# Optimization experiments

Hardware: AMD Instinct MI355X
Metric: run time of the kernel (lower is better)

Reference implementation:

```python
import jax, jax.numpy as jnp
import numpy as np

N_HEAD = 16
N_KV_HEAD = 4
HEAD_DIM = 64
VE_CH = 12  # min(12, n_embd)


def apply_rotary_emb(x, cos, sin):
    d = x.shape[3] // 2
    x1, x2 = x[..., :d], x[..., d:]
    return jnp.concatenate([x1 * cos + x2 * sin, x1 * -sin + x2 * cos], axis=3)


def rms_norm(x):
    return x * jax.lax.rsqrt(jnp.mean(jnp.square(x), axis=-1, keepdims=True) + 1e-6)


def setup_inputs() -> dict:
    key = jax.random.key(0)
    ks = jax.random.split(key, 9)
    B, T, C = 2, 2048, 1024
    s = 0.02
    return {
        "x": jax.random.normal(ks[0], (B, T, C), jnp.float32),
        "ve": jax.random.normal(ks[1], (B, T, N_KV_HEAD * HEAD_DIM), jnp.float32),
        "cos": jax.random.normal(ks[2], (1, T, 1, HEAD_DIM // 2), jnp.float32),
        "sin": jax.random.normal(ks[3], (1, T, 1, HEAD_DIM // 2), jnp.float32),
        "Wq": jax.random.normal(ks[4], (C, C), jnp.float32) * s,
        "Wk": jax.random.normal(ks[5], (N_KV_HEAD * HEAD_DIM, C), jnp.float32) * s,
        "Wv": jax.random.normal(ks[6], (N_KV_HEAD * HEAD_DIM, C), jnp.float32) * s,
        "Wo": jax.random.normal(ks[7], (C, C), jnp.float32) * s,
        "Wg": jax.random.normal(ks[8], (N_KV_HEAD, VE_CH), jnp.float32) * s,
    }


def reference(x, ve, cos, sin, Wq, Wk, Wv, Wo, Wg):
    B, T, C = x.shape
    q = (x @ Wq.T).reshape(B, T, N_HEAD, HEAD_DIM)
    k = (x @ Wk.T).reshape(B, T, N_KV_HEAD, HEAD_DIM)
    v = (x @ Wv.T).reshape(B, T, N_KV_HEAD, HEAD_DIM)

    # value-embedding gate
    ve_r = ve.reshape(B, T, N_KV_HEAD, HEAD_DIM)
    gate = 3.0 * jax.nn.sigmoid(x[..., :VE_CH] @ Wg.T)  # [B,T,n_kv_head]
    v = v + gate[..., None] * ve_r

    q = apply_rotary_emb(q, cos, sin)
    k = apply_rotary_emb(k, cos, sin)
    q = rms_norm(q) * 1.2
    k = rms_norm(k) * 1.2

    # GQA: expand kv heads
    r = N_HEAD // N_KV_HEAD
    k = jnp.repeat(k, r, axis=2)
    v = jnp.repeat(v, r, axis=2)

    # [B,H,T,D]
    q = q.transpose(0, 2, 1, 3)
    k = k.transpose(0, 2, 1, 3)
    v = v.transpose(0, 2, 1, 3)

    scale = 1.0 / np.sqrt(HEAD_DIM).astype(np.float32)
    scores = jnp.einsum("bhqd,bhkd->bhqk", q, k) * scale
    causal = jnp.tril(jnp.ones((T, T), dtype=bool))
    scores = jnp.where(causal, scores, jnp.float32(-jnp.inf))
    att = jax.nn.softmax(scores, axis=-1)
    y = jnp.einsum("bhqk,bhkd->bhqd", att, v)
    y = y.transpose(0, 2, 1, 3).reshape(B, T, C)
    return y @ Wo.T
```

## Files before the change

### kernel.cpp

```cpp
#include <hip/hip_runtime.h>
#include <stdint.h>

#define B_SZ 2
#define T_SZ 2048
#define C_SZ 1024
#define NH   16
#define NKV  4
#define HD   64
#define KVD  256
#define QKV_N 1536

typedef __attribute__((ext_vector_type(8))) short bf16x8;
typedef __attribute__((ext_vector_type(4))) float f32x4;

#define GL(p) ((const __attribute__((address_space(1))) void*)(p))
#define LD(p) ((__attribute__((address_space(3))) void*)(p))

__device__ inline unsigned short f2bf(float f) {
  union { float f; unsigned u; } v; v.f = f;
  unsigned u = v.u;
  unsigned r = (u + 0x7fffu + ((u >> 16) & 1u)) >> 16;
  return (unsigned short)r;
}
__device__ inline unsigned short bftrunc(float f) {
  union { float f; unsigned u; } v; v.f = f;
  return (unsigned short)(v.u >> 16);
}

struct CvtArgs {
  const float *s0, *s1, *s2, *s3, *s4;
  unsigned short *d0, *d1, *d2, *d3, *d4;
  const float *x, *Wg;
  float *gate;
};
__global__ __launch_bounds__(256) void cvt_all(CvtArgs a) {
  int blk = blockIdx.x, tid = threadIdx.x;
  if (blk >= 6656) {
    int idx = (blk - 6656) * 256 + tid;
    int bt = idx >> 2, kh = idx & 3;
    float s = 0.f;
#pragma unroll
    for (int j = 0; j < 12; j++) s += a.x[(size_t)bt * C_SZ + j] * a.Wg[kh * 12 + j];
    a.gate[idx] = 3.f / (1.f + __expf(-s));
    return;
  }
  const float* s; unsigned short* d; int i;
  if      (blk < 4096) { s = a.s0; d = a.d0; i = blk * 256 + tid; }
  else if (blk < 5120) { s = a.s1; d = a.d1; i = (blk - 4096) * 256 + tid; }
  else if (blk < 5376) { s = a.s2; d = a.d2; i = (blk - 5120) * 256 + tid; }
  else if (blk < 5632) { s = a.s3; d = a.d3; i = (blk - 5376) * 256 + tid; }
  else                 { s = a.s4; d = a.d4; i = (blk - 5632) * 256 + tid; }
  float4 f = ((const float4*)s)[i];
  ushort4 o;
  o.x = f2bf(f.x); o.y = f2bf(f.y); o.z = f2bf(f.z); o.w = f2bf(f.w);
  ((ushort4*)d)[i] = o;
}

#define GEMM_PROLOG(A, Bm, K)                                                        \
  __shared__ unsigned short As[2][64 * 64];                                          \
  __shared__ unsigned short Bs[2][128 * 64];                                         \
  int tid  = threadIdx.x;                                                            \
  int lane = tid & 63;                                                               \
  int wave = tid >> 6;                                                               \
  int quad = lane >> 4;                                                              \
  int l16  = lane & 15;                                                              \
  int m0 = blockIdx.y * 64;                                                          \
  int n0 = blockIdx.x * 128;                                                         \
  int wm = (wave & 1) * 32;                                                          \
  int wn = (wave >> 1) * 64;                                                         \
  f32x4 acc[2][4];                                                                   \
  _Pragma("unroll") for (int i = 0; i < 2; i++)                                      \
    _Pragma("unroll") for (int j = 0; j < 4; j++)                                    \
      acc[i][j] = (f32x4){0.f, 0.f, 0.f, 0.f};                                       \
  int lrow = lane >> 3;                                 \
  int lcol = ((lane & 7) ^ lrow) * 8;                 \
  int sA = wave * 16;                                                                \
  int sB = wave * 32;                                                                \
  const unsigned short* aP0 = &A[(size_t)(m0 + sA + lrow) * K + lcol];               \
  const unsigned short* aP1 = aP0 + 8 * (size_t)K;                                   \
  const unsigned short* bP0 = &Bm[(size_t)(n0 + sB + lrow) * K + lcol];              \
  const unsigned short* bP1 = bP0 + 8 * (size_t)K;                                   \
  const unsigned short* bP2 = bP0 + 16 * (size_t)K;                                  \
  const unsigned short* bP3 = bP0 + 24 * (size_t)K;                                  \
  __builtin_amdgcn_global_load_lds(GL(aP0), LD(&As[0][(sA     ) * 64]), 16, 0, 0);   \
  __builtin_amdgcn_global_load_lds(GL(aP1), LD(&As[0][(sA +  8) * 64]), 16, 0, 0);   \
  __builtin_amdgcn_global_load_lds(GL(bP0), LD(&Bs[0][(sB     ) * 64]), 16, 0, 0);   \
  __builtin_amdgcn_global_load_lds(GL(bP1), LD(&Bs[0][(sB +  8) * 64]), 16, 0, 0);   \
  __builtin_amdgcn_global_load_lds(GL(bP2), LD(&Bs[0][(sB + 16) * 64]), 16, 0, 0);   \
  __builtin_amdgcn_global_load_lds(GL(bP3), LD(&Bs[0][(sB + 24) * 64]), 16, 0, 0);   \
  int swz = l16 & 7;                                                                 \
  int nk = K >> 6;                                                                   \
  for (int ki = 0; ki < nk; ki++) {                                                  \
    int cur = ki & 1, nxt = cur ^ 1;                                                 \
    __syncthreads();                                                                 \
    if (ki + 1 < nk) {                                                               \
      int k0 = (ki + 1) << 6;                                                        \
      __builtin_amdgcn_global_load_lds(GL(aP0 + k0), LD(&As[nxt][(sA     ) * 64]), 16, 0, 0); \
      __builtin_amdgcn_global_load_lds(GL(aP1 + k0), LD(&As[nxt][(sA +  8) * 64]), 16, 0, 0); \
      __builtin_amdgcn_global_load_lds(GL(bP0 + k0), LD(&Bs[nxt][(sB     ) * 64]), 16, 0, 0); \
      __builtin_amdgcn_global_load_lds(GL(bP1 + k0), LD(&Bs[nxt][(sB +  8) * 64]), 16, 0, 0); \
      __builtin_amdgcn_global_load_lds(GL(bP2 + k0), LD(&Bs[nxt][(sB + 16) * 64]), 16, 0, 0); \
      __builtin_amdgcn_global_load_lds(GL(bP3 + k0), LD(&Bs[nxt][(sB + 24) * 64]), 16, 0, 0); \
    }                                                                                \
    _Pragma("unroll") for (int p = 0; p < 2; p++) {                                  \
      bf16x8 af[2], bfr[4];                                                          \
      _Pragma("unroll") for (int i = 0; i < 2; i++)                                  \
        af[i] = *(const bf16x8*)&As[cur][(wm + i * 16 + l16) * 64 + (((p * 4 + quad) ^ swz) * 8)]; \
      _Pragma("unroll") for (int j = 0; j < 4; j++)                                  \
        bfr[j] = *(const bf16x8*)&Bs[cur][(wn + j * 16 + l16) * 64 + (((p * 4 + quad) ^ swz) * 8)]; \
      _Pragma("unroll") for (int i = 0; i < 2; i++)                                  \
        _Pragma("unroll") for (int j = 0; j < 4; j++)                                \
          acc[i][j] = __builtin_amdgcn_mfma_f32_16x16x32_bf16(af[i], bfr[j], acc[i][j], 0, 0, 0); \
    }                                                                                \
  }

__global__ __launch_bounds__(256) void gemm_bt(const unsigned short* __restrict__ A,
                                               const unsigned short* __restrict__ Bm,
                                               float* __restrict__ C,
                                               int N, int K) {
  GEMM_PROLOG(A, Bm, K)
#pragma unroll
  for (int i = 0; i < 2; i++) {
#pragma unroll
    for (int j = 0; j < 4; j++) {
      int col = n0 + wn + j * 16 + l16;
#pragma unroll
      for (int r = 0; r < 4; r++) {
        int row = m0 + wm + i * 16 + quad * 4 + r;
        C[(size_t)row * N + col] = acc[i][j][r];
      }
    }
  }
}

__global__ __launch_bounds__(256) void gemm_qkv(const unsigned short* __restrict__ A,
                                                const unsigned short* __restrict__ Bm,
                                                const float* __restrict__ ve,
                                                const float* __restrict__ cosb,
                                                const float* __restrict__ sinb,
                                                const float* __restrict__ gateArr,
                                                unsigned short* __restrict__ qa,
                                                unsigned short* __restrict__ ka,
                                                unsigned short* __restrict__ vt) {
  const int K = C_SZ;
  GEMM_PROLOG(A, Bm, K)

  int colbase = n0 + wn;
  if (colbase < 1280) {
    int isQ = colbase < 1024;
    int h   = isQ ? (colbase >> 6) : ((colbase - 1024) >> 6);
    float scale = isQ ? (0.15f * 1.44269504088896f) : 1.2f;
    unsigned short* dst = isQ ? qa : ka;
    int nheads = isQ ? NH : NKV;
#pragma unroll
    for (int i = 0; i < 2; i++) {
#pragma unroll
      for (int r = 0; r < 4; r++) {
        int row = m0 + wm + i * 16 + quad * 4 + r;
        int t = row & (T_SZ - 1), b = row >> 11;
        float a10 = acc[i][0][r], a11 = acc[i][1][r];
        float a20 = acc[i][2][r], a21 = acc[i][3][r];
        float cv0 = cosb[t * 32 + l16],      sv0 = sinb[t * 32 + l16];
        float cv1 = cosb[t * 32 + 16 + l16], sv1 = sinb[t * 32 + 16 + l16];
        float o10 =  a10 * cv0 + a20 * sv0;
        float o11 =  a11 * cv1 + a21 * sv1;
        float o20 = -a10 * sv0 + a20 * cv0;
        float o21 = -a11 * sv1 + a21 * cv1;
        float ssq = o10 * o10 + o11 * o11 + o20 * o20 + o21 * o21;
        ssq += __shfl_xor(ssq, 1);
        ssq += __shfl_xor(ssq, 2);
        ssq += __shfl_xor(ssq, 4);
        ssq += __shfl_xor(ssq, 8);
        float rn = rsqrtf(ssq * (1.f / 64.f) + 1e-6f) * scale;
        size_t base = ((size_t)(b * nheads + h) * T_SZ + t) * HD;
        dst[base + l16]      = f2bf(o10 * rn);
        dst[base + 16 + l16] = f2bf(o11 * rn);
        dst[base + 32 + l16] = f2bf(o20 * rn);
        dst[base + 48 + l16] = f2bf(o21 * rn);
      }
    }
  } else {
    int kh  = (colbase - 1280) >> 6;
    int khb = (n0 - 1280) >> 6;
    unsigned short* tile = (unsigned short*)&Bs[0][0];
    const int TS = 132;
#pragma unroll
    for (int i = 0; i < 2; i++) {
#pragma unroll
      for (int r = 0; r < 4; r++) {
        int rl  = wm + i * 16 + quad * 4 + r;
        int row = m0 + rl;
        float g = gateArr[row * 4 + kh];
#pragma unroll
        for (int j = 0; j < 4; j++) {
          int d = j * 16 + l16;
          float val = acc[i][j][r] + g * ve[(size_t)row * KVD + kh * HD + d];
          tile[rl * TS + wn + d] = f2bf(val);
        }
      }
    }
    __syncthreads();
    int d2  = tid & 127;
    int seg = tid >> 7;
    int khw = khb + (d2 >> 6);
    int dd  = d2 & 63;
    int bb  = m0 >> 11;
    int tl0 = (m0 & (T_SZ - 1)) + seg * 32;
    unsigned short* dstp = &vt[((size_t)(bb * NKV + khw) * HD + dd) * T_SZ + tl0];
#pragma unroll
    for (int k4 = 0; k4 < 8; k4++) {
      ushort4 o;
      o.x = tile[(seg * 32 + k4 * 4 + 0) * TS + d2];
      o.y = tile[(seg * 32 + k4 * 4 + 1) * TS + d2];
      o.z = tile[(seg * 32 + k4 * 4 + 2) * TS + d2];
      o.w = tile[(seg * 32 + k4 * 4 + 3) * TS + d2];
      *(ushort4*)(dstp + k4 * 4) = o;
    }
  }
}

#define KST 72
#define PST 72
__global__ __launch_bounds__(512, 4) void attn(const unsigned short* __restrict__ qa,
                                               const unsigned short* __restrict__ ka,
                                               const unsigned short* __restrict__ vt,
                                               unsigned short* __restrict__ y) {
  int bid = blockIdx.x;
  int half = bid >> 8, r = bid & 255;
  int qt = half ? (r & 15) : 15 - (r & 15);
  int bh = (half << 4) | (r >> 4);
  int b = bh >> 4, h = bh & 15;
  int kh = h >> 2;
  int tid = threadIdx.x;
  int wave = tid >> 6, lane = tid & 63;
  int quad = lane >> 4, l16 = lane & 15;

  __shared__ unsigned short Ks[2][64 * KST];
  __shared__ unsigned short Vs[2][64 * KST];
  __shared__ unsigned short Ps[128 * PST];
  unsigned short* Pw = &Ps[(wave * 16) * PST];

  int qrow0 = qt * 128 + wave * 16;

  bf16x8 bq0, bq1;
  {
    int tq = qrow0 + l16;
    const unsigned short* qp = &qa[((size_t)(b * NH + h) * T_SZ + tq) * HD];
    bq0 = *(const bf16x8*)&qp[quad * 8];
    bq1 = *(const bf16x8*)&qp[32 + quad * 8];
  }

  const unsigned short one_bf = 0x3F80;
  bf16x8 vones = {(short)one_bf, (short)one_bf, (short)one_bf, (short)one_bf,
                  (short)one_bf, (short)one_bf, (short)one_bf, (short)one_bf};

  f32x4 oacc[4];
  f32x4 lacc = (f32x4){0.f, 0.f, 0.f, 0.f};
#pragma unroll
  for (int d = 0; d < 4; d++) oacc[d] = (f32x4){0.f, 0.f, 0.f, 0.f};

  int lr = tid >> 3;
  int lc = (tid & 7) * 8;

  const unsigned short* kbase = &ka[(size_t)(b * NKV + kh) * T_SZ * HD];
  const unsigned short* vbase = &vt[(size_t)(b * NKV + kh) * HD * T_SZ];

  int nj = 2 * qt + 2;

  {
    uint4 k0 = *(const uint4*)&kbase[(size_t)lr * HD + lc];
    uint4 v0 = *(const uint4*)&vbase[(size_t)lr * T_SZ + lc];
    *(uint4*)&Ks[0][lr * KST + lc] = k0;
    *(uint4*)&Vs[0][lr * KST + lc] = v0;
  }

  for (int j = 0; j < nj; j++) {
    int cur = j & 1, nxt = cur ^ 1;
    __syncthreads();

    uint4 k0, v0;
    bool pf = (j + 1 < nj);
    if (pf) {
      k0 = *(const uint4*)&kbase[(size_t)((j + 1) * 64 + lr) * HD + lc];
      v0 = *(const uint4*)&vbase[(size_t)lr * T_SZ + (j + 1) * 64 + lc];
    }

    bool active = (j * 64) <= (qrow0 + 15);

    if (active) {
      f32x4 st[4];
      __builtin_amdgcn_s_setprio(1);
#pragma unroll
      for (int tb = 0; tb < 4; tb++) {
        bf16x8 ak0 = *(const bf16x8*)&Ks[cur][(tb * 16 + l16) * KST + quad * 8];
        bf16x8 ak1 = *(const bf16x8*)&Ks[cur][(tb * 16 + l16) * KST + 32 + quad * 8];
        f32x4 s = (f32x4){0.f, 0.f, 0.f, 0.f};
        s = __builtin_amdgcn_mfma_f32_16x16x32_bf16(ak0, bq0, s, 0, 0, 0);
        s = __builtin_amdgcn_mfma_f32_16x16x32_bf16(ak1, bq1, s, 0, 0, 0);
        st[tb] = s;
      }
      __builtin_amdgcn_s_setprio(0);

      if (j * 64 + 63 > qrow0) {
        int qg = qrow0 + l16;
#pragma unroll
        for (int tb = 0; tb < 4; tb++) {
          int tg = j * 64 + tb * 16 + quad * 4;
#pragma unroll
          for (int i = 0; i < 4; i++) {
            if (tg + i > qg) st[tb][i] = -__builtin_inff();
          }
        }
      }
#pragma unroll
      for (int tb = 0; tb < 4; tb++) {
        ushort4 w;
        w.x = bftrunc(__builtin_amdgcn_exp2f(st[tb][0]));
        w.y = bftrunc(__builtin_amdgcn_exp2f(st[tb][1]));
        w.z = bftrunc(__builtin_amdgcn_exp2f(st[tb][2]));
        w.w = bftrunc(__builtin_amdgcn_exp2f(st[tb][3]));
        *(ushort4*)&Pw[l16 * PST + tb * 16 + quad * 4] = w;
      }

      bf16x8 ap0 = *(const bf16x8*)&Pw[l16 * PST + quad * 8];
      bf16x8 ap1 = *(const bf16x8*)&Pw[l16 * PST + 32 + quad * 8];
      __builtin_amdgcn_s_setprio(1);
      lacc = __builtin_amdgcn_mfma_f32_16x16x32_bf16(ap0, vones, lacc, 0, 0, 0);
      lacc = __builtin_amdgcn_mfma_f32_16x16x32_bf16(ap1, vones, lacc, 0, 0, 0);
#pragma unroll
      for (int d = 0; d < 4; d++) {
        bf16x8 bv0 = *(const bf16x8*)&Vs[cur][(d * 16 + l16) * KST + quad * 8];
        bf16x8 bv1 = *(const bf16x8*)&Vs[cur][(d * 16 + l16) * KST + 32 + quad * 8];
        oacc[d] = __builtin_amdgcn_mfma_f32_16x16x32_bf16(ap0, bv0, oacc[d], 0, 0, 0);
        oacc[d] = __builtin_amdgcn_mfma_f32_16x16x32_bf16(ap1, bv1, oacc[d], 0, 0, 0);
      }
      __builtin_amdgcn_s_setprio(0);
    }

    if (pf) {
      *(uint4*)&Ks[nxt][lr * KST + lc] = k0;
      *(uint4*)&Vs[nxt][lr * KST + lc] = v0;
    }
  }

#pragma unroll
  for (int i = 0; i < 4; i++) {
    int tq = qrow0 + quad * 4 + i;
    float inv = 1.f / lacc[i];
#pragma unroll
    for (int d = 0; d < 4; d++) {
      y[((size_t)(b * T_SZ) + tq) * C_SZ + h * HD + d * 16 + l16] = f2bf(oacc[d][i] * inv);
    }
  }
}

extern "C" void kernel_launch(void* const* d_in, const int* in_sizes, int n_in,
                              void* d_out, int out_size, void* d_ws, size_t ws_size,
                              hipStream_t stream) {
  const float* x    = (const float*)d_in[0];
  const float* ve   = (const float*)d_in[1];
  const float* cosb = (const float*)d_in[2];
  const float* sinb = (const float*)d_in[3];
  const float* Wq   = (const float*)d_in[4];
  const float* Wk   = (const float*)d_in[5];
  const float* Wv   = (const float*)d_in[6];
  const float* Wo   = (const float*)d_in[7];
  const float* Wg   = (const float*)d_in[8];
  float* out = (float*)d_out;

  const size_t MB = 1024 * 1024;
  char* ws = (char*)d_ws;
  unsigned short* xb    = (unsigned short*)(ws);
  unsigned short* wqkvb = (unsigned short*)(ws + 8 * MB);
  unsigned short* wob   = (unsigned short*)(ws + 11 * MB);
  unsigned short* qab   = (unsigned short*)(ws + 13 * MB);
  unsigned short* kab   = (unsigned short*)(ws + 21 * MB);
  unsigned short* vtb   = (unsigned short*)(ws + 23 * MB);
  float*          gateA = (float*)(ws + 25 * MB);
  unsigned short* yb    = xb;

  CvtArgs ca;
  ca.s0 = x;  ca.d0 = xb;
  ca.s1 = Wq; ca.d1 = wqkvb;
  ca.s2 = Wk; ca.d2 = wqkvb + 1024 * 1024;
  ca.s3 = Wv; ca.d3 = wqkvb + 1280 * 1024;
  ca.s4 = Wo; ca.d4 = wob;
  ca.x = x; ca.Wg = Wg; ca.gate = gateA;
  cvt_all<<<6720, 256, 0, stream>>>(ca);

  gemm_qkv<<<dim3(QKV_N / 128, (B_SZ * T_SZ) / 64), 256, 0, stream>>>(
      xb, wqkvb, ve, cosb, sinb, gateA, qab, kab, vtb);

  attn<<<512, 512, 0, stream>>>(qab, kab, vtb, yb);

  gemm_bt<<<dim3(C_SZ / 128, (B_SZ * T_SZ) / 64), 256, 0, stream>>>(
      yb, wob, out, C_SZ, C_SZ);
}
```

Before: 161.4 us.

## Switch attention to 32x32 MFMA with register-resident P via permlane swap

Rewrites the attention kernel so each wave handles 32 query rows with 32x32x16 bf16 MFMAs instead of 16x16x32. The softmax probabilities stay in registers: they are packed with v_cvt_pk_bf16_f32 and rearranged with v_permlane32_swap, which removes the per-wave LDS round trip for P. The row sum is now accumulated in scalar adds instead of an MFMA against a ones vector. Blocks drop to 256 threads (4 waves) with the same 128-query tile, which raises per-thread register use and removes the occupancy hint.

```diff
diff --git a/kernel.cpp b/kernel.cpp
--- a/kernel.cpp
+++ b/kernel.cpp
@@ -12,6 +12,7 @@
 
 typedef __attribute__((ext_vector_type(8))) short bf16x8;
 typedef __attribute__((ext_vector_type(4))) float f32x4;
+typedef __attribute__((ext_vector_type(16))) float f32x16;
 
 #define GL(p) ((const __attribute__((address_space(1))) void*)(p))
 #define LD(p) ((__attribute__((address_space(3))) void*)(p))
@@ -22,9 +23,10 @@
   unsigned r = (u + 0x7fffu + ((u >> 16) & 1u)) >> 16;
   return (unsigned short)r;
 }
-__device__ inline unsigned short bftrunc(float f) {
-  union { float f; unsigned u; } v; v.f = f;
-  return (unsigned short)(v.u >> 16);
+__device__ inline unsigned cvtpk_bf16(float lo, float hi_) {
+  unsigned r;
+  asm("v_cvt_pk_bf16_f32 %0, %1, %2" : "=v"(r) : "v"(lo), "v"(hi_));
+  return r;
 }
 
 struct CvtArgs {
@@ -220,11 +222,10 @@
 }
 
 #define KST 72
-#define PST 72
-__global__ __launch_bounds__(512, 4) void attn(const unsigned short* __restrict__ qa,
-                                               const unsigned short* __restrict__ ka,
-                                               const unsigned short* __restrict__ vt,
-                                               unsigned short* __restrict__ y) {
+__global__ __launch_bounds__(256) void attn(const unsigned short* __restrict__ qa,
+                                            const unsigned short* __restrict__ ka,
+                                            const unsigned short* __restrict__ vt,
+                                            unsigned short* __restrict__ y) {
   int bid = blockIdx.x;
   int half = bid >> 8, r = bid & 255;
   int qt = half ? (r & 15) : 15 - (r & 15);
@@ -233,34 +234,30 @@
   int kh = h >> 2;
   int tid = threadIdx.x;
   int wave = tid >> 6, lane = tid & 63;
-  int quad = lane >> 4, l16 = lane & 15;
+  int l32 = lane & 31, hi = lane >> 5;
 
   __shared__ unsigned short Ks[2][64 * KST];
   __shared__ unsigned short Vs[2][64 * KST];
-  __shared__ unsigned short Ps[128 * PST];
-  unsigned short* Pw = &Ps[(wave * 16) * PST];
-
-  int qrow0 = qt * 128 + wave * 16;
-
-  bf16x8 bq0, bq1;
+  __shared__ float Ls[4][32];
+
+  int qrow0 = qt * 128 + wave * 32;
+
+  bf16x8 bq[4];
   {
-    int tq = qrow0 + l16;
-    const unsigned short* qp = &qa[((size_t)(b * NH + h) * T_SZ + tq) * HD];
-    bq0 = *(const bf16x8*)&qp[quad * 8];
-    bq1 = *(const bf16x8*)&qp[32 + quad * 8];
-  }
-
-  const unsigned short one_bf = 0x3F80;
-  bf16x8 vones = {(short)one_bf, (short)one_bf, (short)one_bf, (short)one_bf,
-                  (short)one_bf, (short)one_bf, (short)one_bf, (short)one_bf};
-
-  f32x4 oacc[4];
-  f32x4 lacc = (f32x4){0.f, 0.f, 0.f, 0.f};
-#pragma unroll
-  for (int d = 0; d < 4; d++) oacc[d] = (f32x4){0.f, 0.f, 0.f, 0.f};
-
-  int lr = tid >> 3;
-  int lc = (tid & 7) * 8;
+    const unsigned short* qp = &qa[((size_t)(b * NH + h) * T_SZ + qrow0 + l32) * HD + hi * 8];
+    bq[0] = *(const bf16x8*)(qp);
+    bq[1] = *(const bf16x8*)(qp + 16);
+    bq[2] = *(const bf16x8*)(qp + 32);
+    bq[3] = *(const bf16x8*)(qp + 48);
+  }
+
+  f32x16 oacc0, oacc1;
+#pragma unroll
+  for (int i = 0; i < 16; i++) { oacc0[i] = 0.f; oacc1[i] = 0.f; }
+  float lsum = 0.f;
+
+  int lr   = tid >> 2;
+  int gcol = (tid & 3) * 16;
 
   const unsigned short* kbase = &ka[(size_t)(b * NKV + kh) * T_SZ * HD];
   const unsigned short* vbase = &vt[(size_t)(b * NKV + kh) * HD * T_SZ];
@@ -268,88 +265,121 @@
   int nj = 2 * qt + 2;
 
   {
-    uint4 k0 = *(const uint4*)&kbase[(size_t)lr * HD + lc];
-    uint4 v0 = *(const uint4*)&vbase[(size_t)lr * T_SZ + lc];
-    *(uint4*)&Ks[0][lr * KST + lc] = k0;
-    *(uint4*)&Vs[0][lr * KST + lc] = v0;
+    uint4 k0 = *(const uint4*)&kbase[(size_t)lr * HD + gcol];
+    uint4 k1 = *(const uint4*)&kbase[(size_t)lr * HD + gcol + 8];
+    uint4 v0 = *(const uint4*)&vbase[(size_t)lr * T_SZ + gcol];
+    uint4 v1 = *(const uint4*)&vbase[(size_t)lr * T_SZ + gcol + 8];
+    *(uint4*)&Ks[0][lr * KST + gcol]     = k0;
+    *(uint4*)&Ks[0][lr * KST + gcol + 8] = k1;
+    *(uint4*)&Vs[0][lr * KST + gcol]     = v0;
+    *(uint4*)&Vs[0][lr * KST + gcol + 8] = v1;
   }
 
   for (int j = 0; j < nj; j++) {
     int cur = j & 1, nxt = cur ^ 1;
     __syncthreads();
 
-    uint4 k0, v0;
+    uint4 k0, k1, v0, v1;
     bool pf = (j + 1 < nj);
     if (pf) {
-      k0 = *(const uint4*)&kbase[(size_t)((j + 1) * 64 + lr) * HD + lc];
-      v0 = *(const uint4*)&vbase[(size_t)lr * T_SZ + (j + 1) * 64 + lc];
-    }
-
-    bool active = (j * 64) <= (qrow0 + 15);
-
+      k0 = *(const uint4*)&kbase[(size_t)((j + 1) * 64 + lr) * HD + gcol];
+      k1 = *(const uint4*)&kbase[(size_t)((j + 1) * 64 + lr) * HD + gcol + 8];
+      v0 = *(const uint4*)&vbase[(size_t)lr * T_SZ + (j + 1) * 64 + gcol];
+      v1 = *(const uint4*)&vbase[(size_t)lr * T_SZ + (j + 1) * 64 + gcol + 8];
+    }
+
+    bool active = (j * 64) <= (qrow0 + 31);
     if (active) {
-      f32x4 st[4];
+      f32x16 st0, st1;
+#pragma unroll
+      for (int i = 0; i < 16; i++) { st0[i] = 0.f; st1[i] = 0.f; }
       __builtin_amdgcn_s_setprio(1);
 #pragma unroll
-      for (int tb = 0; tb < 4; tb++) {
-        bf16x8 ak0 = *(const bf16x8*)&Ks[cur][(tb * 16 + l16) * KST + quad * 8];
-        bf16x8 ak1 = *(const bf16x8*)&Ks[cur][(tb * 16 + l16) * KST + 32 + quad * 8];
-        f32x4 s = (f32x4){0.f, 0.f, 0.f, 0.f};
-        s = __builtin_amdgcn_mfma_f32_16x16x32_bf16(ak0, bq0, s, 0, 0, 0);
-        s = __builtin_amdgcn_mfma_f32_16x16x32_bf16(ak1, bq1, s, 0, 0, 0);
-        st[tb] = s;
+      for (int kc = 0; kc < 4; kc++) {
+        bf16x8 ak0 = *(const bf16x8*)&Ks[cur][(l32)      * KST + kc * 16 + hi * 8];
+        bf16x8 ak1 = *(const bf16x8*)&Ks[cur][(32 + l32) * KST + kc * 16 + hi * 8];
+        st0 = __builtin_amdgcn_mfma_f32_32x32x16_bf16(ak0, bq[kc], st0, 0, 0, 0);
+        st1 = __builtin_amdgcn_mfma_f32_32x32x16_bf16(ak1, bq[kc], st1, 0, 0, 0);
       }
       __builtin_amdgcn_s_setprio(0);
 
       if (j * 64 + 63 > qrow0) {
-        int qg = qrow0 + l16;
-#pragma unroll
-        for (int tb = 0; tb < 4; tb++) {
-          int tg = j * 64 + tb * 16 + quad * 4;
-#pragma unroll
-          for (int i = 0; i < 4; i++) {
-            if (tg + i > qg) st[tb][i] = -__builtin_inff();
-          }
+        int qg = qrow0 + l32;
+#pragma unroll
+        for (int rg = 0; rg < 16; rg++) {
+          int t0r = j * 64 + (rg & 3) + 8 * (rg >> 2) + 4 * hi;
+          if (t0r > qg)      st0[rg] = -__builtin_inff();
+          if (t0r + 32 > qg) st1[rg] = -__builtin_inff();
         }
       }
-#pragma unroll
-      for (int tb = 0; tb < 4; tb++) {
-        ushort4 w;
-        w.x = bftrunc(__builtin_amdgcn_exp2f(st[tb][0]));
-        w.y = bftrunc(__builtin_amdgcn_exp2f(st[tb][1]));
-        w.z = bftrunc(__builtin_amdgcn_exp2f(st[tb][2]));
-        w.w = bftrunc(__builtin_amdgcn_exp2f(st[tb][3]));
-        *(ushort4*)&Pw[l16 * PST + tb * 16 + quad * 4] = w;
-      }
-
-      bf16x8 ap0 = *(const bf16x8*)&Pw[l16 * PST + quad * 8];
-      bf16x8 ap1 = *(const bf16x8*)&Pw[l16 * PST + 32 + quad * 8];
+
+#pragma unroll
+      for (int rg = 0; rg < 16; rg++) {
+        st0[rg] = __builtin_amdgcn_exp2f(st0[rg]);
+        st1[rg] = __builtin_amdgcn_exp2f(st1[rg]);
+        lsum += st0[rg] + st1[rg];
+      }
+
+      union { unsigned u[4]; bf16x8 v; } pa[4];
+#pragma unroll
+      for (int sub = 0; sub < 2; sub++) {
+        unsigned L0m0 = cvtpk_bf16(sub ? st1[0]  : st0[0],  sub ? st1[1]  : st0[1]);
+        unsigned L0m1 = cvtpk_bf16(sub ? st1[2]  : st0[2],  sub ? st1[3]  : st0[3]);
+        unsigned L1m0 = cvtpk_bf16(sub ? st1[4]  : st0[4],  sub ? st1[5]  : st0[5]);
+        unsigned L1m1 = cvtpk_bf16(sub ? st1[6]  : st0[6],  sub ? st1[7]  : st0[7]);
+        unsigned L2m0 = cvtpk_bf16(sub ? st1[8]  : st0[8],  sub ? st1[9]  : st0[9]);
+        unsigned L2m1 = cvtpk_bf16(sub ? st1[10] : st0[10], sub ? st1[11] : st0[11]);
+        unsigned L3m0 = cvtpk_bf16(sub ? st1[12] : st0[12], sub ? st1[13] : st0[13]);
+        unsigned L3m1 = cvtpk_bf16(sub ? st1[14] : st0[14], sub ? st1[15] : st0[15]);
+        asm("v_permlane32_swap_b32 %0, %1" : "+v"(L0m0), "+v"(L1m0));
+        asm("v_permlane32_swap_b32 %0, %1" : "+v"(L0m1), "+v"(L1m1));
+        asm("v_permlane32_swap_b32 %0, %1" : "+v"(L2m0), "+v"(L3m0));
+        asm("v_permlane32_swap_b32 %0, %1" : "+v"(L2m1), "+v"(L3m1));
+        pa[sub * 2 + 0].u[0] = L0m0; pa[sub * 2 + 0].u[1] = L0m1;
+        pa[sub * 2 + 0].u[2] = L1m0; pa[sub * 2 + 0].u[3] = L1m1;
+        pa[sub * 2 + 1].u[0] = L2m0; pa[sub * 2 + 1].u[1] = L2m1;
+        pa[sub * 2 + 1].u[2] = L3m0; pa[sub * 2 + 1].u[3] = L3m1;
+      }
+
       __builtin_amdgcn_s_setprio(1);
-      lacc = __builtin_amdgcn_mfma_f32_16x16x32_bf16(ap0, vones, lacc, 0, 0, 0);
-      lacc = __builtin_amdgcn_mfma_f32_16x16x32_bf16(ap1, vones, lacc, 0, 0, 0);
-#pragma unroll
-      for (int d = 0; d < 4; d++) {
-        bf16x8 bv0 = *(const bf16x8*)&Vs[cur][(d * 16 + l16) * KST + quad * 8];
-        bf16x8 bv1 = *(const bf16x8*)&Vs[cur][(d * 16 + l16) * KST + 32 + quad * 8];
-        oacc[d] = __builtin_amdgcn_mfma_f32_16x16x32_bf16(ap0, bv0, oacc[d], 0, 0, 0);
-        oacc[d] = __builtin_amdgcn_mfma_f32_16x16x32_bf16(ap1, bv1, oacc[d], 0, 0, 0);
+#pragma unroll
+      for (int c = 0; c < 4; c++) {
+        bf16x8 bv0 = *(const bf16x8*)&Vs[cur][(l32)      * KST + c * 16 + hi * 8];
+        bf16x8 bv1 = *(const bf16x8*)&Vs[cur][(32 + l32) * KST + c * 16 + hi * 8];
+        oacc0 = __builtin_amdgcn_mfma_f32_32x32x16_bf16(pa[c].v, bv0, oacc0, 0, 0, 0);
+        oacc1 = __builtin_amdgcn_mfma_f32_32x32x16_bf16(pa[c].v, bv1, oacc1, 0, 0, 0);
       }
       __builtin_amdgcn_s_setprio(0);
     }
 
     if (pf) {
-      *(uint4*)&Ks[nxt][lr * KST + lc] = k0;
-      *(uint4*)&Vs[nxt][lr * KST + lc] = v0;
-    }
-  }
-
-#pragma unroll
-  for (int i = 0; i < 4; i++) {
-    int tq = qrow0 + quad * 4 + i;
-    float inv = 1.f / lacc[i];
-#pragma unroll
-    for (int d = 0; d < 4; d++) {
-      y[((size_t)(b * T_SZ) + tq) * C_SZ + h * HD + d * 16 + l16] = f2bf(oacc[d][i] * inv);
+      *(uint4*)&Ks[nxt][lr * KST + gcol]     = k0;
+      *(uint4*)&Ks[nxt][lr * KST + gcol + 8] = k1;
+      *(uint4*)&Vs[nxt][lr * KST + gcol]     = v0;
+      *(uint4*)&Vs[nxt][lr * KST + gcol + 8] = v1;
+    }
+  }
+
+  {
+    union { float f; unsigned u; } a, bcp;
+    a.f = lsum; bcp.f = lsum;
+    asm("v_permlane32_swap_b32 %0, %1" : "+v"(a.u), "+v"(bcp.u));
+    float total = a.f + bcp.f;
+    if (hi == 0) Ls[wave][l32] = total;
+  }
+  __syncthreads();
+
+#pragma unroll
+  for (int g = 0; g < 4; g++) {
+    f32x4 tv = *(const f32x4*)&Ls[wave][8 * g + 4 * hi];
+#pragma unroll
+    for (int i = 0; i < 4; i++) {
+      int rg = 4 * g + i;
+      int tq = qrow0 + 8 * g + 4 * hi + i;
+      float inv = 1.f / tv[i];
+      unsigned short* yp = &y[((size_t)(b * T_SZ) + tq) * C_SZ + h * HD + l32];
+      yp[0]  = f2bf(oacc0[rg] * inv);
+      yp[32] = f2bf(oacc1[rg] * inv);
     }
   }
 }
@@ -391,7 +421,7 @@
   gemm_qkv<<<dim3(QKV_N / 128, (B_SZ * T_SZ) / 64), 256, 0, stream>>>(
       xb, wqkvb, ve, cosb, sinb, gateA, qab, kab, vtb);
 
-  attn<<<512, 512, 0, stream>>>(qab, kab, vtb, yb);
+  attn<<<512, 256, 0, stream>>>(qab, kab, vtb, yb);
 
   gemm_bt<<<dim3(C_SZ / 128, (B_SZ * T_SZ) / 64), 256, 0, stream>>>(
       yb, wob, out, C_SZ, C_SZ);
```

Measured after the change: 164.0 us. About the same (+1.7%).
